# Kernel tuning notes

Hardware: AMD Instinct MI355X
Metric: run time of the kernel (lower is better)

Reference implementation:

```python
import jax, jax.numpy as jnp
import numpy as np

D_MODEL = 2048
N_HEADS = 8
EXPAND_K = 1
EXPAND_V = 2
DK = D_MODEL * EXPAND_K // N_HEADS      # 256 per-head key dim
DV = D_MODEL * EXPAND_V // N_HEADS      # 512 per-head value dim
INTER = 5632
EPS = 1e-6
CHUNK = 64


def setup_inputs() -> dict:
    key = jax.random.key(0)
    ks = jax.random.split(key, 12)
    d = D_MODEL
    s = lambda fan_in: 1.0 / np.sqrt(fan_in)
    return {
        "hidden_states": jax.random.normal(ks[0], (2, 2048, d), jnp.float32),
        "attn_norm_w": jnp.ones((d,), jnp.float32),
        "q_w": jax.random.normal(ks[1], (d, d * EXPAND_K), jnp.float32) * s(d),
        "k_w": jax.random.normal(ks[2], (d, d * EXPAND_K), jnp.float32) * s(d),
        "v_w": jax.random.normal(ks[3], (d, d * EXPAND_V), jnp.float32) * s(d),
        "g_w": jax.random.normal(ks[4], (d, d * EXPAND_V), jnp.float32) * s(d),
        "o_w": jax.random.normal(ks[5], (d * EXPAND_V, d), jnp.float32) * s(d * EXPAND_V),
        "gnorm_w": jnp.ones((DV,), jnp.float32),
        "mlp_norm_w": jnp.ones((d,), jnp.float32),
        "gate_w": jax.random.normal(ks[6], (d, INTER * 2), jnp.float32) * s(d),
        "down_w": jax.random.normal(ks[7], (INTER, d), jnp.float32) * s(INTER),
    }


def rmsnorm(x, w, eps=EPS):
    return x * jax.lax.rsqrt(jnp.mean(x * x, axis=-1, keepdims=True) + eps) * w


def rope(x):
    # x: [B, T, H, D]; non-interleaved rotary on full head dim
    T, D = x.shape[1], x.shape[-1]
    inv_freq = 1.0 / (10000.0 ** (jnp.arange(0, D, 2, dtype=jnp.float32) / D))
    ang = jnp.arange(T, dtype=jnp.float32)[:, None] * inv_freq  # [T, D/2]
    cos = jnp.cos(ang)[None, :, None, :]
    sin = jnp.sin(ang)[None, :, None, :]
    x1, x2 = jnp.split(x, 2, axis=-1)
    return jnp.concatenate([x1 * cos - x2 * sin, x2 * cos + x1 * sin], axis=-1)


def chunk_retention(q, k, v):
    # q,k: [B,T,H,Dk], v: [B,T,H,Dv]; chunkwise-recurrent RetNet retention
    B, T, H, Dk = q.shape
    Dv = v.shape[-1]
    C = CHUNK
    N = T // C
    gamma = 1.0 - jnp.exp2(-5.0 - jnp.arange(H, dtype=jnp.float32))  # [H]
    i = jnp.arange(C, dtype=jnp.float32)
    diff = i[:, None] - i[None, :]
    Dmask = jnp.where(diff >= 0, gamma[:, None, None] ** diff, 0.0)   # [H,C,C]
    cross_decay = gamma[:, None] ** (i[None, :] + 1.0)                # [H,C]
    k_decay = gamma[:, None] ** (C - 1.0 - i[None, :])                # [H,C]
    chunk_decay = gamma ** C                                          # [H]

    # -> [N, B, H, C, D]
    to_chunks = lambda x: jnp.moveaxis(
        x.reshape(B, N, C, H, x.shape[-1]).transpose(0, 1, 3, 2, 4), 1, 0)
    qc, kc, vc = to_chunks(q), to_chunks(k), to_chunks(v)

    def body(S, inp):
        qb, kb, vb = inp  # [B,H,C,Dk/Dv]
        attn = jnp.einsum('bhid,bhjd->bhij', qb, kb) * Dmask
        o_intra = jnp.einsum('bhij,bhje->bhie', attn, vb)
        o_cross = jnp.einsum('bhid,bhde->bhie', qb * cross_decay[None, :, :, None], S)
        S = chunk_decay[None, :, None, None] * S + \
            jnp.einsum('bhid,bhie->bhde', kb * k_decay[None, :, :, None], vb)
        return S, o_intra + o_cross

    S0 = jnp.zeros((B, H, Dk, Dv), q.dtype)
    _, o = jax.lax.scan(body, S0, (qc, kc, vc))  # o: [N,B,H,C,Dv]
    return jnp.moveaxis(o, 0, 1).transpose(0, 1, 3, 2, 4).reshape(B, T, H, Dv)


def reference(hidden_states, attn_norm_w, q_w, k_w, v_w, g_w, o_w, gnorm_w,
              mlp_norm_w, gate_w, down_w):
    B, T, d = hidden_states.shape
    residual = hidden_states
    h = rmsnorm(hidden_states, attn_norm_w)

    # MultiScaleRetention
    q = (h @ q_w).reshape(B, T, N_HEADS, DK)
    k = (h @ k_w).reshape(B, T, N_HEADS, DK)
    v = (h @ v_w).reshape(B, T, N_HEADS, DV)
    g = (h @ g_w).reshape(B, T, N_HEADS, DV)
    q, k = rope(q), rope(k)
    q = q * (DK ** -0.5)
    o = chunk_retention(q, k, v)
    # fused RMSNorm + swish gate (per head over Dv)
    o = rmsnorm(o, gnorm_w) * (g * jax.nn.sigmoid(g))
    h = o.reshape(B, T, N_HEADS * DV) @ o_w

    # fused-residual RMSNorm
    residual = h + residual
    h = rmsnorm(residual, mlp_norm_w)

    # SwiGLU MLP
    y = h @ gate_w
    gate, y = jnp.split(y, 2, axis=-1)
    h = (gate * jax.nn.sigmoid(gate) * y) @ down_w
    return residual + h
```

## Files before the change

kernel.cpp:

```cpp
#include <hip/hip_runtime.h>
#include <cstdint>
#include <cstddef>

typedef unsigned short u16;
typedef __attribute__((ext_vector_type(4))) float f32x4;
typedef __attribute__((ext_vector_type(4))) unsigned int u32x4;

__device__ __forceinline__ float b2f(u16 u) {
  union { unsigned int i; float f; } x; x.i = ((unsigned int)u) << 16; return x.f;
}
__device__ __forceinline__ u16 f2b(float f) {
  union { float f; unsigned int i; } x; x.f = f;
  unsigned int i = x.i;
  i += 0x7fffu + ((i >> 16) & 1u);
  return (u16)(i >> 16);
}

__device__ __forceinline__ void mfma_bf16(f32x4& c, u32x4 a, u32x4 b) {
  asm("v_mfma_f32_16x16x32_bf16 %0, %1, %2, %0" : "+v"(c) : "v"(a), "v"(b));
}

__device__ __forceinline__ void async_ld16(const u16* g, u16* l) {
  typedef __attribute__((address_space(1))) const unsigned int GU;
  typedef __attribute__((address_space(3))) unsigned int LU;
  __builtin_amdgcn_global_load_lds((GU*)g, (LU*)l, 16, 0, 0);
}

__global__ __launch_bounds__(256)
void transpose_cast_kernel(const float* __restrict__ in, u16* __restrict__ out,
                           int K, int N, int ldin) {
  __shared__ float tile[64][65];
  const int nb = N >> 6;
  const int bk = blockIdx.x / nb, bn = blockIdx.x % nb;
  const int k0 = bk * 64, n0 = bn * 64;
  const int tid = threadIdx.x;
#pragma unroll
  for (int p = 0; p < 16; ++p) {
    int idx = p * 256 + tid;
    int r = idx >> 6, c = idx & 63;
    tile[r][c] = in[(size_t)(k0 + r) * ldin + n0 + c];
  }
  __syncthreads();
#pragma unroll
  for (int p = 0; p < 16; ++p) {
    int idx = p * 256 + tid;
    int r = idx >> 6, c = idx & 63;
    out[(size_t)(n0 + r) * K + k0 + c] = f2b(tile[c][r]);
  }
}

__global__ __launch_bounds__(256)
void transpose_k_kernel(const u16* __restrict__ kb, u16* __restrict__ kt) {
  __shared__ u16 tile[64][72];
  const int bid = blockIdx.x;
  const int dd = bid & 3, tt = (bid >> 2) & 31;
  const int h = (bid >> 7) & 7, b = bid >> 10;
  const int t0 = tt * 64, d0 = dd * 64;
  const int tid = threadIdx.x;
#pragma unroll
  for (int p = 0; p < 2; ++p) {
    int idx = p * 256 + tid;
    int r = idx >> 3, cq = (idx & 7) * 8;
    *(uint4*)&tile[r][cq] =
        *(const uint4*)&kb[(size_t)(b * 2048 + t0 + r) * 2048 + h * 256 + d0 + cq];
  }
  __syncthreads();
#pragma unroll
  for (int p = 0; p < 2; ++p) {
    int idx = p * 256 + tid;
    int r = idx >> 3, cq = (idx & 7) * 8;
    union { u16 h8[8]; uint4 v4; } o;
#pragma unroll
    for (int j = 0; j < 8; ++j) o.h8[j] = tile[cq + j][r];
    *(uint4*)&kt[((size_t)(b * 8 + h) * 256 + d0 + r) * 2048 + t0 + cq] = o.v4;
  }
}

__global__ __launch_bounds__(256)
void rmsnorm_cast_kernel(const float* __restrict__ x, const float* __restrict__ w,
                         u16* __restrict__ out) {
  const int row = blockIdx.x, tid = threadIdx.x;
  const float* xr = x + (size_t)row * 2048;
  float4 a = ((const float4*)xr)[tid * 2];
  float4 b = ((const float4*)xr)[tid * 2 + 1];
  float ss = a.x*a.x + a.y*a.y + a.z*a.z + a.w*a.w
           + b.x*b.x + b.y*b.y + b.z*b.z + b.w*b.w;
#pragma unroll
  for (int m = 32; m; m >>= 1) ss += __shfl_xor(ss, m);
  __shared__ float ps[4];
  if ((tid & 63) == 0) ps[tid >> 6] = ss;
  __syncthreads();
  const float sc = rsqrtf((ps[0] + ps[1] + ps[2] + ps[3]) * (1.0f / 2048.0f) + 1e-6f);
  const int base = tid * 8;
  const float vals[8] = {a.x, a.y, a.z, a.w, b.x, b.y, b.z, b.w};
  union { u16 h[8]; uint4 v4[2]; } o;
#pragma unroll
  for (int j = 0; j < 8; ++j) o.h[j] = f2b(vals[j] * sc * w[base + j]);
  *(uint4*)&out[(size_t)row * 2048 + base] = o.v4[0];
  *(uint4*)&out[(size_t)row * 2048 + base + 8] = o.v4[1];
}

__global__ __launch_bounds__(256)
void rmsnorm_bf16_kernel(const u16* __restrict__ x, const float* __restrict__ w,
                         u16* __restrict__ out) {
  const int row = blockIdx.x, tid = threadIdx.x;
  union { uint4 v4; u16 h[8]; } p;
  p.v4 = *(const uint4*)&x[(size_t)row * 2048 + tid * 8];
  float v[8];
  float ss = 0.f;
#pragma unroll
  for (int j = 0; j < 8; ++j) { v[j] = b2f(p.h[j]); ss += v[j] * v[j]; }
#pragma unroll
  for (int m = 32; m; m >>= 1) ss += __shfl_xor(ss, m);
  __shared__ float ps[4];
  if ((tid & 63) == 0) ps[tid >> 6] = ss;
  __syncthreads();
  const float sc = rsqrtf((ps[0] + ps[1] + ps[2] + ps[3]) * (1.0f / 2048.0f) + 1e-6f);
  union { u16 h[8]; uint4 v4; } o;
#pragma unroll
  for (int j = 0; j < 8; ++j) o.h[j] = f2b(v[j] * sc * w[tid * 8 + j]);
  *(uint4*)&out[(size_t)row * 2048 + tid * 8] = o.v4;
}

__global__ __launch_bounds__(256)
void rope_table_kernel(float* __restrict__ ct, float* __restrict__ st) {
  const int idx = blockIdx.x * 256 + threadIdx.x;
  const int t = idx >> 7, i = idx & 127;
  const float e = -(float)i * (0.0078125f * log2f(10000.0f));
  const float ang = (float)t * exp2f(e);
  ct[idx] = cosf(ang);
  st[idx] = sinf(ang);
}

__global__ __launch_bounds__(256)
void rope_apply_kernel(u16* __restrict__ x, const float* __restrict__ ct,
                       const float* __restrict__ st, float scale) {
  const int gid = blockIdx.x * 256 + threadIdx.x;
  const int r = gid >> 8;
  const int rem = gid & 255;
  const int h = rem >> 5;
  const int i4 = (rem & 31) * 4;
  const int t = r & 2047;
  const size_t o1 = (size_t)r * 2048 + h * 256 + i4;
  union { ushort4 v; u16 h4[4]; } p1, p2, q1, q2;
  p1.v = *(ushort4*)&x[o1];
  p2.v = *(ushort4*)&x[o1 + 128];
  const float4 c = *(const float4*)&ct[t * 128 + i4];
  const float4 s = *(const float4*)&st[t * 128 + i4];
  const float cc[4] = {c.x, c.y, c.z, c.w};
  const float sn[4] = {s.x, s.y, s.z, s.w};
#pragma unroll
  for (int j = 0; j < 4; ++j) {
    float x1 = b2f(p1.h4[j]), x2 = b2f(p2.h4[j]);
    q1.h4[j] = f2b((x1 * cc[j] - x2 * sn[j]) * scale);
    q2.h4[j] = f2b((x2 * cc[j] + x1 * sn[j]) * scale);
  }
  *(ushort4*)&x[o1] = q1.v;
  *(ushort4*)&x[o1 + 128] = q2.v;
}

template <int EPI>
__global__ __launch_bounds__(256, 2)
void gemm_bt(const u16* __restrict__ A, const u16* __restrict__ Bt,
             void* Cout, const float* fsrc, const u16* hsrc, int N, int K) {
  __shared__ __align__(16) u16 As[128 * 32];
  __shared__ __align__(16) u16 Bs[128 * 32];
  const int tid = threadIdx.x;
  const int l = tid & 63, w = tid >> 6;
  const int lr = l & 15, hi = l >> 4;
  const int nbn = N >> 7;
  const int bm = blockIdx.x / nbn, bn = blockIdx.x % nbn;
  const int f0 = w * 512 + l * 8;
  const int r0 = f0 >> 5, c0 = f0 & 31;
  const u16* ga0 = A + (size_t)(bm * 128 + r0) * K + c0;
  const u16* ga1 = ga0 + (size_t)64 * K;
  const u16* gb0 = Bt + (size_t)(bn * 128 + r0) * K + c0;
  const u16* gb1 = gb0 + (size_t)64 * K;
  u16* la = As + w * 512;
  u16* lb = Bs + w * 512;
  f32x4 acc[4][4];
#pragma unroll
  for (int m = 0; m < 4; ++m)
#pragma unroll
    for (int n = 0; n < 4; ++n) acc[m][n] = (f32x4){0.f, 0.f, 0.f, 0.f};
  const int wr = (w >> 1) * 64, wc = (w & 1) * 64;
  for (int k0 = 0; k0 < K; k0 += 32) {
    async_ld16(ga0 + k0, la);
    async_ld16(ga1 + k0, la + 2048);
    async_ld16(gb0 + k0, lb);
    async_ld16(gb1 + k0, lb + 2048);
    __syncthreads();
    u32x4 af[4], bfr[4];
#pragma unroll
    for (int m = 0; m < 4; ++m)
      af[m] = *(const u32x4*)&As[(wr + m * 16 + lr) * 32 + hi * 8];
#pragma unroll
    for (int n = 0; n < 4; ++n)
      bfr[n] = *(const u32x4*)&Bs[(wc + n * 16 + lr) * 32 + hi * 8];
#pragma unroll
    for (int m = 0; m < 4; ++m)
#pragma unroll
      for (int n = 0; n < 4; ++n) mfma_bf16(acc[m][n], af[m], bfr[n]);
    __syncthreads();
  }
  const size_t crow0 = (size_t)(bm * 128 + wr);
  const int ccol0 = bn * 128 + wc;
#pragma unroll
  for (int m = 0; m < 4; ++m)
#pragma unroll
    for (int n = 0; n < 4; ++n)
#pragma unroll
      for (int j = 0; j < 4; ++j) {
        size_t r = crow0 + m * 16 + hi * 4 + j;
        size_t c = (size_t)(ccol0 + n * 16 + lr);
        size_t idx = r * N + c;
        float a = acc[m][n][j];
        if (EPI == 1) {
          ((u16*)Cout)[idx] = f2b(a);
        } else if (EPI == 2) {
          ((float*)Cout)[idx] = a + b2f(hsrc[idx]);
        } else if (EPI == 3) {
          float u = b2f(hsrc[idx]);
          ((u16*)Cout)[idx] = f2b(a / (1.0f + expf(-a)) * u);
        } else {
          ((u16*)Cout)[idx] = f2b(a + fsrc[idx]);
        }
      }
}

#define LGK 264
#define LGC 72
__global__ __launch_bounds__(512)
void retention_kernel(const u16* __restrict__ q, const u16* __restrict__ k,
                      const u16* __restrict__ kt, const u16* __restrict__ v,
                      u16* __restrict__ o) {
  __shared__ __align__(16) u16 ks[64 * LGK];
  __shared__ __align__(16) u16 stb[32 * LGK];
  __shared__ __align__(16) u16 ktd[256 * LGC];
  __shared__ __align__(16) u16 vts[32 * LGC];
  __shared__ __align__(16) u16 ab[64 * LGC];
  __shared__ float kdt[64];

  const int tid = threadIdx.x;
  const int l = tid & 63, w = tid >> 6;
  const int lr = l & 15, hi = l >> 4;
  const int wr = w >> 1;
  const int eb = w & 1;
  const int bid = blockIdx.x;
  const int sl = bid & 15;
  const int hh = (bid >> 4) & 7;
  const int b = bid >> 7;
  const float gamma = 1.0f - exp2f(-5.0f - (float)hh);
  const float lg = log2f(gamma);
  const float cdk = exp2f(64.0f * lg);
  const int e0 = sl * 32;

  if (tid < 64) kdt[tid] = exp2f((float)(63 - tid) * lg);
  __syncthreads();

  f32x4 st[4];
#pragma unroll
  for (int t = 0; t < 4; ++t) st[t] = (f32x4){0.f, 0.f, 0.f, 0.f};

  for (int n = 0; n < 32; ++n) {
    const int row0 = b * 2048 + n * 64;
    const int t0 = n * 64;
#pragma unroll
    for (int t = 0; t < 4; ++t)
#pragma unroll
      for (int j = 0; j < 4; ++j)
        stb[(eb * 16 + hi * 4 + j) * LGK + (wr * 4 + t) * 16 + lr] = f2b(st[t][j]);
    u32x4 qf[8];
#pragma unroll
    for (int kk = 0; kk < 8; ++kk)
      qf[kk] = *(const u32x4*)&q[(size_t)(row0 + wr * 16 + lr) * 2048 +
                                 hh * 256 + kk * 32 + hi * 8];
#pragma unroll
    for (int p = 0; p < 4; ++p) {
      int idx = p * 512 + tid;
      int c = idx >> 5, s = (idx & 31) * 8;
      *(uint4*)&ks[c * LGK + s] =
          *(const uint4*)&k[(size_t)(row0 + c) * 2048 + hh * 256 + s];
    }
#pragma unroll
    for (int p = 0; p < 4; ++p) {
      int idx = p * 512 + tid;
      int d = idx >> 3, cq = (idx & 7) * 8;
      union { uint4 v4; u16 h[8]; } pk;
      pk.v4 = *(const uint4*)&kt[((size_t)(b * 8 + hh) * 256 + d) * 2048 + t0 + cq];
      union { u16 h[8]; uint4 v4; } wo;
#pragma unroll
      for (int j2 = 0; j2 < 8; ++j2)
        wo.h[j2] = f2b(b2f(pk.h[j2]) * kdt[cq + j2]);
      *(uint4*)&ktd[d * LGC + cq] = wo.v4;
    }
#pragma unroll
    for (int p = 0; p < 4; ++p) {
      int c = (tid >> 5) + p * 16, e = tid & 31;
      vts[e * LGC + c] = v[(size_t)(row0 + c) * 4096 + hh * 512 + e0 + e];
    }
    __syncthreads();

    f32x4 att[2];
    att[0] = (f32x4){0.f, 0.f, 0.f, 0.f};
    att[1] = (f32x4){0.f, 0.f, 0.f, 0.f};
#pragma unroll
    for (int kk = 0; kk < 8; ++kk) {
#pragma unroll
      for (int jf = 0; jf < 2; ++jf) {
        u32x4 bb = *(const u32x4*)&ks[(eb * 32 + jf * 16 + lr) * LGK + kk * 32 + hi * 8];
        mfma_bf16(att[jf], qf[kk], bb);
      }
    }
#pragma unroll
    for (int jf = 0; jf < 2; ++jf)
#pragma unroll
      for (int j = 0; j < 4; ++j) {
        int i = wr * 16 + hi * 4 + j;
        int jc = eb * 32 + jf * 16 + lr;
        float mv = (i >= jc) ? exp2f((float)(i - jc) * lg) : 0.0f;
        ab[i * LGC + jc] = f2b(att[jf][j] * mv);
      }
    f32x4 occ = (f32x4){0.f, 0.f, 0.f, 0.f};
#pragma unroll
    for (int kk = 0; kk < 8; ++kk) {
      u32x4 bb = *(const u32x4*)&stb[(eb * 16 + lr) * LGK + kk * 32 + hi * 8];
      mfma_bf16(occ, qf[kk], bb);
    }
    __syncthreads();

#pragma unroll
    for (int j = 0; j < 4; ++j) {
      int i = wr * 16 + hi * 4 + j;
      occ[j] *= exp2f((float)(i + 1) * lg);
    }
#pragma unroll
    for (int kk = 0; kk < 2; ++kk) {
      u32x4 aa = *(const u32x4*)&ab[(wr * 16 + lr) * LGC + kk * 32 + hi * 8];
      u32x4 bb = *(const u32x4*)&vts[(eb * 16 + lr) * LGC + kk * 32 + hi * 8];
      mfma_bf16(occ, aa, bb);
    }
#pragma unroll
    for (int j = 0; j < 4; ++j) {
      int i = wr * 16 + hi * 4 + j;
      o[(size_t)(row0 + i) * 4096 + hh * 512 + e0 + eb * 16 + lr] = f2b(occ[j]);
    }
#pragma unroll
    for (int t = 0; t < 4; ++t) {
      st[t][0] *= cdk; st[t][1] *= cdk; st[t][2] *= cdk; st[t][3] *= cdk;
    }
#pragma unroll
    for (int kk = 0; kk < 2; ++kk) {
      u32x4 aa = *(const u32x4*)&vts[(eb * 16 + lr) * LGC + kk * 32 + hi * 8];
#pragma unroll
      for (int t = 0; t < 4; ++t) {
        u32x4 bb = *(const u32x4*)&ktd[((wr * 4 + t) * 16 + lr) * LGC + kk * 32 + hi * 8];
        mfma_bf16(st[t], aa, bb);
      }
    }
    __syncthreads();
  }
}

__global__ __launch_bounds__(64)
void gating_kernel(u16* __restrict__ o, const u16* __restrict__ g,
                   const float* __restrict__ gnw) {
  const int blk = blockIdx.x;
  const size_t base = (size_t)blk * 512;
  const int l = threadIdx.x;
  union { uint4 v4; u16 h[8]; } ov, gv;
  ov.v4 = *(const uint4*)&o[base + l * 8];
  float x[8];
  float ss = 0.f;
#pragma unroll
  for (int j = 0; j < 8; ++j) { x[j] = b2f(ov.h[j]); ss += x[j] * x[j]; }
#pragma unroll
  for (int m = 32; m; m >>= 1) ss += __shfl_xor(ss, m);
  const float sc = rsqrtf(ss * (1.0f / 512.0f) + 1e-6f);
  gv.v4 = *(const uint4*)&g[base + l * 8];
  union { u16 h[8]; uint4 v4; } ou;
#pragma unroll
  for (int j = 0; j < 8; ++j) {
    float gvf = b2f(gv.h[j]);
    float sig = 1.0f / (1.0f + expf(-gvf));
    ou.h[j] = f2b(x[j] * sc * gnw[l * 8 + j] * gvf * sig);
  }
  *(uint4*)&o[base + l * 8] = ou.v4;
}

extern "C" void kernel_launch(void* const* d_in, const int* in_sizes, int n_in,
                              void* d_out, int out_size, void* d_ws, size_t ws_size,
                              hipStream_t stream) {
  (void)in_sizes; (void)n_in; (void)out_size; (void)ws_size;
  const float* hidden      = (const float*)d_in[0];
  const float* attn_norm_w = (const float*)d_in[1];
  const float* q_w         = (const float*)d_in[2];
  const float* k_w         = (const float*)d_in[3];
  const float* v_w         = (const float*)d_in[4];
  const float* g_w         = (const float*)d_in[5];
  const float* o_w         = (const float*)d_in[6];
  const float* gnorm_w     = (const float*)d_in[7];
  const float* mlp_norm_w  = (const float*)d_in[8];
  const float* gate_w      = (const float*)d_in[9];
  const float* down_w      = (const float*)d_in[10];
  float* outp = (float*)d_out;

  char* ws = (char*)d_ws;
  size_t off = 0;
  auto alloc = [&](size_t bytes) -> char* {
    char* p = ws + off;
    off += (bytes + 255) & ~(size_t)255;
    return p;
  };
  u16*   W    = (u16*)alloc(23068672ULL);
  float* ctab = (float*)alloc(1048576ULL);
  float* stab = (float*)alloc(1048576ULL);
  u16*   hb   = (u16*)alloc(16777216ULL);
  u16*   qb   = (u16*)alloc(16777216ULL);
  u16*   kb   = (u16*)alloc(16777216ULL);
  u16*   vb   = (u16*)alloc(33554432ULL);
  u16*   gb   = (u16*)alloc(33554432ULL);
  u16*   ob   = (u16*)alloc(33554432ULL);
  u16*   resb = (u16*)alloc(16777216ULL);
  u16*   ybU  = vb;
  u16*   kt   = W;

  rope_table_kernel<<<1024, 256, 0, stream>>>(ctab, stab);
  rmsnorm_cast_kernel<<<4096, 256, 0, stream>>>(hidden, attn_norm_w, hb);

  transpose_cast_kernel<<<1024, 256, 0, stream>>>(q_w, W, 2048, 2048, 2048);
  gemm_bt<1><<<512, 256, 0, stream>>>(hb, W, (void*)qb, nullptr, nullptr, 2048, 2048);
  transpose_cast_kernel<<<1024, 256, 0, stream>>>(k_w, W, 2048, 2048, 2048);
  gemm_bt<1><<<512, 256, 0, stream>>>(hb, W, (void*)kb, nullptr, nullptr, 2048, 2048);
  transpose_cast_kernel<<<2048, 256, 0, stream>>>(v_w, W, 2048, 4096, 4096);
  gemm_bt<1><<<1024, 256, 0, stream>>>(hb, W, (void*)vb, nullptr, nullptr, 4096, 2048);
  transpose_cast_kernel<<<2048, 256, 0, stream>>>(g_w, W, 2048, 4096, 4096);
  gemm_bt<1><<<1024, 256, 0, stream>>>(hb, W, (void*)gb, nullptr, nullptr, 4096, 2048);

  rope_apply_kernel<<<4096, 256, 0, stream>>>(qb, ctab, stab, 0.0625f);
  rope_apply_kernel<<<4096, 256, 0, stream>>>(kb, ctab, stab, 1.0f);
  transpose_k_kernel<<<2048, 256, 0, stream>>>(kb, kt);

  retention_kernel<<<256, 512, 0, stream>>>(qb, kb, kt, vb, ob);

  gating_kernel<<<32768, 64, 0, stream>>>(ob, gb, gnorm_w);

  transpose_cast_kernel<<<2048, 256, 0, stream>>>(o_w, W, 4096, 2048, 2048);
  gemm_bt<4><<<512, 256, 0, stream>>>(ob, W, (void*)resb, hidden, nullptr, 2048, 4096);

  rmsnorm_bf16_kernel<<<4096, 256, 0, stream>>>(resb, mlp_norm_w, hb);

  transpose_cast_kernel<<<2816, 256, 0, stream>>>(gate_w + 5632, W, 2048, 5632, 11264);
  gemm_bt<1><<<1408, 256, 0, stream>>>(hb, W, (void*)ybU, nullptr, nullptr, 5632, 2048);
  transpose_cast_kernel<<<2816, 256, 0, stream>>>(gate_w, W, 2048, 5632, 11264);
  gemm_bt<3><<<1408, 256, 0, stream>>>(hb, W, (void*)ybU, nullptr, ybU, 5632, 2048);

  transpose_cast_kernel<<<2816, 256, 0, stream>>>(down_w, W, 5632, 2048, 2048);
  gemm_bt<2><<<512, 256, 0, stream>>>(ybU, W, (void*)outp, nullptr, resb, 2048, 5632);
}
```

Baseline: 1.040 ms.

## Swizzle GEMM LDS layout, remap blocks across XCDs, fuse Q/K projection GEMM

```diff
diff --git a/kernel.cpp b/kernel.cpp
--- a/kernel.cpp
+++ b/kernel.cpp
@@ -5,6 +5,7 @@
 typedef unsigned short u16;
 typedef __attribute__((ext_vector_type(4))) float f32x4;
 typedef __attribute__((ext_vector_type(4))) unsigned int u32x4;
+typedef __attribute__((ext_vector_type(8))) short s16x8;
 
 __device__ __forceinline__ float b2f(u16 u) {
   union { unsigned int i; float f; } x; x.i = ((unsigned int)u) << 16; return x.f;
@@ -17,7 +18,9 @@
 }
 
 __device__ __forceinline__ void mfma_bf16(f32x4& c, u32x4 a, u32x4 b) {
-  asm("v_mfma_f32_16x16x32_bf16 %0, %1, %2, %0" : "+v"(c) : "v"(a), "v"(b));
+  union { u32x4 u; s16x8 s; } ua, ub;
+  ua.u = a; ub.u = b;
+  c = __builtin_amdgcn_mfma_f32_16x16x32_bf16(ua.s, ub.s, c, 0, 0, 0);
 }
 
 __device__ __forceinline__ void async_ld16(const u16* g, u16* l) {
@@ -50,7 +53,7 @@
 }
 
 __global__ __launch_bounds__(256)
-void transpose_k_kernel(const u16* __restrict__ kb, u16* __restrict__ kt) {
+void transpose_k_kernel(const u16* __restrict__ qk, u16* __restrict__ kt) {
   __shared__ u16 tile[64][72];
   const int bid = blockIdx.x;
   const int dd = bid & 3, tt = (bid >> 2) & 31;
@@ -62,7 +65,7 @@
     int idx = p * 256 + tid;
     int r = idx >> 3, cq = (idx & 7) * 8;
     *(uint4*)&tile[r][cq] =
-        *(const uint4*)&kb[(size_t)(b * 2048 + t0 + r) * 2048 + h * 256 + d0 + cq];
+        *(const uint4*)&qk[(size_t)(b * 2048 + t0 + r) * 4096 + 2048 + h * 256 + d0 + cq];
   }
   __syncthreads();
 #pragma unroll
@@ -134,14 +137,14 @@
 
 __global__ __launch_bounds__(256)
 void rope_apply_kernel(u16* __restrict__ x, const float* __restrict__ ct,
-                       const float* __restrict__ st, float scale) {
+                       const float* __restrict__ st, int qoff, float scale) {
   const int gid = blockIdx.x * 256 + threadIdx.x;
   const int r = gid >> 8;
   const int rem = gid & 255;
   const int h = rem >> 5;
   const int i4 = (rem & 31) * 4;
   const int t = r & 2047;
-  const size_t o1 = (size_t)r * 2048 + h * 256 + i4;
+  const size_t o1 = (size_t)r * 4096 + qoff + h * 256 + i4;
   union { ushort4 v; u16 h4[4]; } p1, p2, q1, q2;
   p1.v = *(ushort4*)&x[o1];
   p2.v = *(ushort4*)&x[o1 + 128];
@@ -160,61 +163,78 @@
 }
 
 template <int EPI>
-__global__ __launch_bounds__(256, 2)
-void gemm_bt(const u16* __restrict__ A, const u16* __restrict__ Bt,
-             void* Cout, const float* fsrc, const u16* hsrc, int N, int K) {
-  __shared__ __align__(16) u16 As[128 * 32];
-  __shared__ __align__(16) u16 Bs[128 * 32];
+__global__ __launch_bounds__(256, 3)
+void gemm5(const u16* __restrict__ A, const u16* __restrict__ Bt,
+           void* Cout, const float* fsrc, const u16* hsrc,
+           int N, int K, int lda) {
+  __shared__ __align__(16) char smem[16384];
   const int tid = threadIdx.x;
   const int l = tid & 63, w = tid >> 6;
   const int lr = l & 15, hi = l >> 4;
+  const int wm = w >> 1, wn = w & 1;
+  const int cpx = (int)gridDim.x >> 3;
+  const int bid = (blockIdx.x & 7) * cpx + ((int)blockIdx.x >> 3);
   const int nbn = N >> 7;
-  const int bm = blockIdx.x / nbn, bn = blockIdx.x % nbn;
-  const int f0 = w * 512 + l * 8;
-  const int r0 = f0 >> 5, c0 = f0 & 31;
-  const u16* ga0 = A + (size_t)(bm * 128 + r0) * K + c0;
-  const u16* ga1 = ga0 + (size_t)64 * K;
-  const u16* gb0 = Bt + (size_t)(bn * 128 + r0) * K + c0;
-  const u16* gb1 = gb0 + (size_t)64 * K;
-  u16* la = As + w * 512;
-  u16* lb = Bs + w * 512;
+  const int bm = bid / nbn, bn = bid % nbn;
+  const int nt = K >> 5;
+
+  const u16* Ap[2]; const u16* Bp[2];
+#pragma unroll
+  for (int t = 0; t < 2; ++t) {
+    int s = t * 256 + tid;
+    int row = s >> 2, ch = (s & 3) ^ ((s >> 3) & 3);
+    Ap[t] = A + (size_t)(bm * 128 + row) * lda + ch * 8;
+    Bp[t] = Bt + (size_t)(bn * 128 + row) * K + ch * 8;
+  }
+  const int dst0 = (0 * 256 + w * 64) * 16;
+  const int dst1 = (1 * 256 + w * 64) * 16;
+
+  int aoff[4], boff[4];
+#pragma unroll
+  for (int f = 0; f < 4; ++f) {
+    int ra = wm * 64 + f * 16 + lr;
+    aoff[f] = (ra * 4 + (hi ^ ((ra >> 1) & 3))) * 16;
+    int rb = wn * 64 + f * 16 + lr;
+    boff[f] = 8192 + (rb * 4 + (hi ^ ((rb >> 1) & 3))) * 16;
+  }
+
   f32x4 acc[4][4];
 #pragma unroll
   for (int m = 0; m < 4; ++m)
 #pragma unroll
     for (int n = 0; n < 4; ++n) acc[m][n] = (f32x4){0.f, 0.f, 0.f, 0.f};
-  const int wr = (w >> 1) * 64, wc = (w & 1) * 64;
-  for (int k0 = 0; k0 < K; k0 += 32) {
-    async_ld16(ga0 + k0, la);
-    async_ld16(ga1 + k0, la + 2048);
-    async_ld16(gb0 + k0, lb);
-    async_ld16(gb1 + k0, lb + 2048);
+
+  for (int i = 0; i < nt; ++i) {
+    const int k0 = i * 32;
+    async_ld16(Ap[0] + k0, (u16*)(smem + dst0));
+    async_ld16(Ap[1] + k0, (u16*)(smem + dst1));
+    async_ld16(Bp[0] + k0, (u16*)(smem + 8192 + dst0));
+    async_ld16(Bp[1] + k0, (u16*)(smem + 8192 + dst1));
     __syncthreads();
-    u32x4 af[4], bfr[4];
+    u32x4 af[4], bf[4];
+#pragma unroll
+    for (int f = 0; f < 4; ++f) af[f] = *(const u32x4*)(smem + aoff[f]);
+#pragma unroll
+    for (int f = 0; f < 4; ++f) bf[f] = *(const u32x4*)(smem + boff[f]);
 #pragma unroll
     for (int m = 0; m < 4; ++m)
-      af[m] = *(const u32x4*)&As[(wr + m * 16 + lr) * 32 + hi * 8];
+#pragma unroll
+      for (int n = 0; n < 4; ++n) mfma_bf16(acc[m][n], af[m], bf[n]);
+    __syncthreads();
+  }
+
+  const size_t crow0 = (size_t)(bm * 128 + wm * 64);
+  const int ccol0 = bn * 128 + wn * 64;
+#pragma unroll
+  for (int m = 0; m < 4; ++m)
 #pragma unroll
     for (int n = 0; n < 4; ++n)
-      bfr[n] = *(const u32x4*)&Bs[(wc + n * 16 + lr) * 32 + hi * 8];
-#pragma unroll
-    for (int m = 0; m < 4; ++m)
-#pragma unroll
-      for (int n = 0; n < 4; ++n) mfma_bf16(acc[m][n], af[m], bfr[n]);
-    __syncthreads();
-  }
-  const size_t crow0 = (size_t)(bm * 128 + wr);
-  const int ccol0 = bn * 128 + wc;
-#pragma unroll
-  for (int m = 0; m < 4; ++m)
-#pragma unroll
-    for (int n = 0; n < 4; ++n)
-#pragma unroll
-      for (int j = 0; j < 4; ++j) {
-        size_t r = crow0 + m * 16 + hi * 4 + j;
+#pragma unroll
+      for (int j2 = 0; j2 < 4; ++j2) {
+        size_t r = crow0 + m * 16 + hi * 4 + j2;
         size_t c = (size_t)(ccol0 + n * 16 + lr);
         size_t idx = r * N + c;
-        float a = acc[m][n][j];
+        float a = acc[m][n][j2];
         if (EPI == 1) {
           ((u16*)Cout)[idx] = f2b(a);
         } else if (EPI == 2) {
@@ -231,9 +251,8 @@
 #define LGK 264
 #define LGC 72
 __global__ __launch_bounds__(512)
-void retention_kernel(const u16* __restrict__ q, const u16* __restrict__ k,
-                      const u16* __restrict__ kt, const u16* __restrict__ v,
-                      u16* __restrict__ o) {
+void retention_kernel(const u16* __restrict__ qk, const u16* __restrict__ kt,
+                      const u16* __restrict__ v, u16* __restrict__ o) {
   __shared__ __align__(16) u16 ks[64 * LGK];
   __shared__ __align__(16) u16 stb[32 * LGK];
   __shared__ __align__(16) u16 ktd[256 * LGC];
@@ -247,9 +266,10 @@
   const int wr = w >> 1;
   const int eb = w & 1;
   const int bid = blockIdx.x;
-  const int sl = bid & 15;
-  const int hh = (bid >> 4) & 7;
-  const int b = bid >> 7;
+  const int g = bid & 15;
+  const int sl = bid >> 4;
+  const int hh = g & 7;
+  const int b = g >> 3;
   const float gamma = 1.0f - exp2f(-5.0f - (float)hh);
   const float lg = log2f(gamma);
   const float cdk = exp2f(64.0f * lg);
@@ -273,14 +293,14 @@
     u32x4 qf[8];
 #pragma unroll
     for (int kk = 0; kk < 8; ++kk)
-      qf[kk] = *(const u32x4*)&q[(size_t)(row0 + wr * 16 + lr) * 2048 +
-                                 hh * 256 + kk * 32 + hi * 8];
+      qf[kk] = *(const u32x4*)&qk[(size_t)(row0 + wr * 16 + lr) * 4096 +
+                                  hh * 256 + kk * 32 + hi * 8];
 #pragma unroll
     for (int p = 0; p < 4; ++p) {
       int idx = p * 512 + tid;
       int c = idx >> 5, s = (idx & 31) * 8;
       *(uint4*)&ks[c * LGK + s] =
-          *(const uint4*)&k[(size_t)(row0 + c) * 2048 + hh * 256 + s];
+          *(const uint4*)&qk[(size_t)(row0 + c) * 4096 + 2048 + hh * 256 + s];
     }
 #pragma unroll
     for (int p = 0; p < 4; ++p) {
@@ -416,45 +436,43 @@
   float* ctab = (float*)alloc(1048576ULL);
   float* stab = (float*)alloc(1048576ULL);
   u16*   hb   = (u16*)alloc(16777216ULL);
-  u16*   qb   = (u16*)alloc(16777216ULL);
-  u16*   kb   = (u16*)alloc(16777216ULL);
+  u16*   qkb  = (u16*)alloc(33554432ULL);
   u16*   vb   = (u16*)alloc(33554432ULL);
   u16*   gb   = (u16*)alloc(33554432ULL);
   u16*   ob   = (u16*)alloc(33554432ULL);
   u16*   resb = (u16*)alloc(16777216ULL);
-  u16*   ybU  = vb;
+  u16*   ybU  = qkb;
   u16*   kt   = W;
 
   rope_table_kernel<<<1024, 256, 0, stream>>>(ctab, stab);
   rmsnorm_cast_kernel<<<4096, 256, 0, stream>>>(hidden, attn_norm_w, hb);
 
   transpose_cast_kernel<<<1024, 256, 0, stream>>>(q_w, W, 2048, 2048, 2048);
-  gemm_bt<1><<<512, 256, 0, stream>>>(hb, W, (void*)qb, nullptr, nullptr, 2048, 2048);
-  transpose_cast_kernel<<<1024, 256, 0, stream>>>(k_w, W, 2048, 2048, 2048);
-  gemm_bt<1><<<512, 256, 0, stream>>>(hb, W, (void*)kb, nullptr, nullptr, 2048, 2048);
+  transpose_cast_kernel<<<1024, 256, 0, stream>>>(k_w, W + 2048ULL * 2048, 2048, 2048, 2048);
+  gemm5<1><<<1024, 256, 0, stream>>>(hb, W, (void*)qkb, nullptr, nullptr, 4096, 2048, 2048);
   transpose_cast_kernel<<<2048, 256, 0, stream>>>(v_w, W, 2048, 4096, 4096);
-  gemm_bt<1><<<1024, 256, 0, stream>>>(hb, W, (void*)vb, nullptr, nullptr, 4096, 2048);
+  gemm5<1><<<1024, 256, 0, stream>>>(hb, W, (void*)vb, nullptr, nullptr, 4096, 2048, 2048);
   transpose_cast_kernel<<<2048, 256, 0, stream>>>(g_w, W, 2048, 4096, 4096);
-  gemm_bt<1><<<1024, 256, 0, stream>>>(hb, W, (void*)gb, nullptr, nullptr, 4096, 2048);
-
-  rope_apply_kernel<<<4096, 256, 0, stream>>>(qb, ctab, stab, 0.0625f);
-  rope_apply_kernel<<<4096, 256, 0, stream>>>(kb, ctab, stab, 1.0f);
-  transpose_k_kernel<<<2048, 256, 0, stream>>>(kb, kt);
-
-  retention_kernel<<<256, 512, 0, stream>>>(qb, kb, kt, vb, ob);
+  gemm5<1><<<1024, 256, 0, stream>>>(hb, W, (void*)gb, nullptr, nullptr, 4096, 2048, 2048);
+
+  rope_apply_kernel<<<4096, 256, 0, stream>>>(qkb, ctab, stab, 0, 0.0625f);
+  rope_apply_kernel<<<4096, 256, 0, stream>>>(qkb, ctab, stab, 2048, 1.0f);
+  transpose_k_kernel<<<2048, 256, 0, stream>>>(qkb, kt);
+
+  retention_kernel<<<256, 512, 0, stream>>>(qkb, kt, vb, ob);
 
   gating_kernel<<<32768, 64, 0, stream>>>(ob, gb, gnorm_w);
 
   transpose_cast_kernel<<<2048, 256, 0, stream>>>(o_w, W, 4096, 2048, 2048);
-  gemm_bt<4><<<512, 256, 0, stream>>>(ob, W, (void*)resb, hidden, nullptr, 2048, 4096);
+  gemm5<4><<<512, 256, 0, stream>>>(ob, W, (void*)resb, hidden, nullptr, 2048, 4096, 4096);
 
   rmsnorm_bf16_kernel<<<4096, 256, 0, stream>>>(resb, mlp_norm_w, hb);
 
   transpose_cast_kernel<<<2816, 256, 0, stream>>>(gate_w + 5632, W, 2048, 5632, 11264);
-  gemm_bt<1><<<1408, 256, 0, stream>>>(hb, W, (void*)ybU, nullptr, nullptr, 5632, 2048);
+  gemm5<1><<<1408, 256, 0, stream>>>(hb, W, (void*)ybU, nullptr, nullptr, 5632, 2048, 2048);
   transpose_cast_kernel<<<2816, 256, 0, stream>>>(gate_w, W, 2048, 5632, 11264);
-  gemm_bt<3><<<1408, 256, 0, stream>>>(hb, W, (void*)ybU, nullptr, ybU, 5632, 2048);
+  gemm5<3><<<1408, 256, 0, stream>>>(hb, W, (void*)ybU, nullptr, ybU, 5632, 2048, 2048);
 
   transpose_cast_kernel<<<2816, 256, 0, stream>>>(down_w, W, 5632, 2048, 2048);
-  gemm_bt<2><<<512, 256, 0, stream>>>(ybU, W, (void*)outp, nullptr, resb, 2048, 5632);
-}
+  gemm5<2><<<512, 256, 0, stream>>>(ybU, W, (void*)outp, nullptr, resb, 2048, 5632, 5632);
+}
```

Result: faster. 984.7 us (-5.3%).
